# Kernel optimization log

Hardware: AMD Instinct MI355X
Metric: run time of the kernel (lower is better)

The kernel has to match this reference:

```python
import jax, jax.numpy as jnp
import numpy as np

LOG_EPS = 1e-30
MIN_EPS = 1e-8
N_CLASS = 19
GAMMA = 1.0        # focal_gamma
ADAPT_B = 0.2
ADAPT_A = 0.9      # beta (a_decay == 0)
ADAPT_D = 8.0
CONF_THRESH = 0.8  # uda_confidence_thresh


def setup_inputs() -> dict:
    key = jax.random.key(0)
    k1, k2 = jax.random.split(key)
    N, C, H, W = 2, N_CLASS, 512, 1024
    logits_before = jax.random.normal(k1, (N, C, H, W), jnp.float32)
    logits_after = jax.random.normal(k2, (N, C, H, W), jnp.float32)
    cls_thresh = jnp.ones((N_CLASS,), jnp.float32) * CONF_THRESH
    return {"logits_before": logits_before, "logits_after": logits_after,
            "cls_thresh": cls_thresh}


def ias_thresh(conf, label, cls_thresh):
    # conf, label: [N,H,W] max-prob and argmax class per pixel
    conf_f = conf.reshape(-1)    # [T]
    label_f = label.reshape(-1)  # [T]

    def per_class(c, thr):
        # class-c confidences, others pushed to the end of the descending sort
        vals = jnp.where(label_f == c, conf_f, -jnp.inf)
        ext = jnp.concatenate([vals, thr[None]])  # append current threshold
        srt = -jnp.sort(-ext)                     # descending
        count = jnp.sum(label_f == c)
        # index = int(len_extend * adapt_b * thresh**adapt_d); len_extend = count+1
        idx = jnp.floor((count + 1).astype(jnp.float32) * ADAPT_B * thr ** ADAPT_D).astype(jnp.int32)
        return srt[idx]  # count==0 -> idx==0 -> picks thr (matches torch branch)

    return jax.vmap(per_class)(jnp.arange(N_CLASS), cls_thresh)


def reference(logits_before, logits_after, cls_thresh):
    pb = jax.nn.softmax(logits_before, axis=1)
    pa = jax.nn.softmax(logits_after, axis=1)
    pb_d = jax.lax.stop_gradient(pb)
    log_pb_d = jnp.log(pb_d + LOG_EPS)
    log_pa = jnp.log(pa + LOG_EPS)

    bma = 1.0 - pa  # focal_type == 1: ones_like(pb_d) - pa
    label = jnp.argmax(pb_d, axis=1)  # [N,H,W]
    conf = jnp.max(pb_d, axis=1)      # [N,H,W]
    # scatter(select_mask)+sum == gather the argmax channel
    sel_diff = jnp.take_along_axis(bma, label[:, None], axis=1)  # [N,1,H,W]

    loss_kldiv = pb_d * (log_pb_d - jnp.abs(sel_diff) ** GAMMA * log_pa)
    loss_entropy = -pb * jnp.log(pb + LOG_EPS)
    loss = jnp.sum(loss_kldiv + loss_entropy, axis=1)  # [N,H,W]

    tmp = ias_thresh(conf, label, cls_thresh)
    new_thresh = ADAPT_A * cls_thresh + (1.0 - ADAPT_A) * tmp
    new_thresh = jnp.where(new_thresh >= 1.0, 0.999, new_thresh)

    pix_thresh = new_thresh[label]           # [N,H,W]
    mask = conf > pix_thresh
    adapt_ratio = jnp.mean(mask.astype(jnp.float32))
    solid_ratio = jnp.mean((conf > CONF_THRESH).astype(jnp.float32))

    # loss[mask] -> clamp -> mean, expressed as a masked mean (jit-safe)
    num = jnp.sum(jnp.where(mask, jnp.maximum(loss, MIN_EPS), 0.0))
    den = jnp.maximum(jnp.sum(mask).astype(loss.dtype), 1.0)
    return num / den, adapt_ratio, solid_ratio
```

## Files before the change

### kernel.cpp

```cpp
#include <hip/hip_runtime.h>
#include <math.h>

#define NCLS 19
#define HW   (512*1024)
#define CHW  (NCLS*HW)
#define TPIX (2*HW)
#define NB   512
#define NPART 32
#define CAND_MAX 4096
#define SUBB 1024
#define SCAP 256

#define WS_PART   0
#define WS_CANDC  622592
#define WS_ACCUM  622720
#define WS_DONE   622784
#define WS_SEL    622848
#define WS_NEWTH  623360
#define WS_CONF   623616
#define WS_LOSS   4817920
#define WS_LABEL  9012224
#define WS_CAND   10060800

#define TILE 256
__global__ __launch_bounds__(256)
void k1_pixel(const float* __restrict__ lb_t, const float* __restrict__ la_t,
              float* __restrict__ conf_o, float* __restrict__ loss_o,
              unsigned char* __restrict__ label_o,
              unsigned int* __restrict__ cand_cnt,
              unsigned int* __restrict__ accum_u,
              unsigned int* __restrict__ done)
{
    __shared__ float smem[2 * NCLS * TILE];
    const int tid = threadIdx.x;
    if (blockIdx.x == 0) {
        if (tid < NCLS)            cand_cnt[tid] = 0u;
        else if (tid < NCLS + 3)   accum_u[tid - NCLS] = 0u;
        else if (tid < NCLS + 6)   done[tid - NCLS - 3] = 0u;
    }
    const int wave = tid >> 6, lane = tid & 63;
    const int tb  = blockIdx.x * TILE;
    const int n   = tb >> 19;
    const int rem = tb & (HW - 1);
    const float* lb = lb_t + (size_t)n * CHW + rem;
    const float* la = la_t + (size_t)n * CHW + rem;

#pragma unroll
    for (int i = 0; i < 10; ++i) {
        int r = wave + 4 * i;
        if (r < 2 * NCLS) {
            const float* src = (r < NCLS) ? (lb + (size_t)r * HW)
                                          : (la + (size_t)(r - NCLS) * HW);
            __builtin_amdgcn_global_load_lds(
                (__attribute__((address_space(1))) void*)(src + (lane << 2)),
                (__attribute__((address_space(3))) void*)(smem + r * TILE),
                16, 0, 0);
        }
    }
    asm volatile("s_waitcnt vmcnt(0)" ::: "memory");
    __syncthreads();

    const int pix = tb + tid;
    float mb, zb, dot, a_lab, ma, za; int lab;
    {
        float bb = smem[tid];
        float aa = smem[NCLS * TILE + tid];
        mb = bb; zb = 1.0f; dot = aa; lab = 0; a_lab = aa; ma = aa; za = 1.0f;
    }
#pragma unroll
    for (int c = 1; c < NCLS; ++c) {
        float b = smem[c * TILE + tid];
        float a = smem[(NCLS + c) * TILE + tid];
        float mn = fmaxf(mb, b);
        float eo = __expf(mb - mn);
        float en = __expf(b - mn);
        zb  = zb * eo + en;
        dot = dot * eo + en * a;
        bool upd = b > mb;
        lab   = upd ? c : lab;
        a_lab = upd ? a : a_lab;
        mb = mn;
        float mna = fmaxf(ma, a);
        za = za * __expf(ma - mna) + __expf(a - mna);
        ma = mna;
    }

    float cf = 1.0f / zb;
    float pa_lab = __expf(a_lab - ma) / za;
    float ls = (1.0f - pa_lab) * (ma + __logf(za) - dot / zb);

    conf_o[pix]  = cf;
    loss_o[pix]  = ls;
    label_o[pix] = (unsigned char)lab;
}

__global__ __launch_bounds__(512)
void k2_hist(const float4* __restrict__ conf, const uchar4* __restrict__ label,
             unsigned short* __restrict__ part)
{
    __shared__ unsigned int lh[NCLS * NB];
    const int t = threadIdx.x;
    for (int w = t; w < NCLS * NB; w += 512) lh[w] = 0u;
    __syncthreads();

    const int per4  = TPIX / 4 / NPART;
    const int base4 = blockIdx.x * per4;
    for (int i = 0; i < per4 / 512; ++i) {
        int g = base4 + i * 512 + t;
        float4 c4 = conf[g];
        uchar4 l4 = label[g];
        float cf[4] = {c4.x, c4.y, c4.z, c4.w};
        int   lb[4] = {l4.x, l4.y, l4.z, l4.w};
#pragma unroll
        for (int k = 0; k < 4; ++k) {
            int bin = (int)(cf[k] * (float)NB);
            bin = bin < (NB - 1) ? bin : (NB - 1);
            atomicAdd(&lh[lb[k] * NB + bin], 1u);
        }
    }
    __syncthreads();

    unsigned short* dst = part + blockIdx.x * (NCLS * NB);
    for (int w = t; w < NCLS * NB; w += 512) dst[w] = (unsigned short)lh[w];
}

__global__ __launch_bounds__(256)
void k2_select(const unsigned short* __restrict__ part, const float* __restrict__ cls_thresh,
               int* __restrict__ sel, unsigned int* __restrict__ cand_cnt,
               float* __restrict__ cand)
{
    int c = blockIdx.x;
    int t = threadIdx.x;
    float thr = cls_thresh[c];
    int thr_bin = (int)(thr * (float)NB); thr_bin = thr_bin < (NB-1) ? thr_bin : (NB-1);

    int base = NB - (t + 1) * 2;
    unsigned h0 = 0, h1 = 0;
#pragma unroll 8
    for (int b = 0; b < NPART; ++b) {
        const unsigned short* p = part + b * (NCLS * NB) + c * NB;
        h0 += p[base];
        h1 += p[base + 1];
    }
    if (base == thr_bin)     h0 += 1u;
    if (base + 1 == thr_bin) h1 += 1u;
    unsigned s = h0 + h1;

    __shared__ unsigned sc[256];
    sc[t] = s;
    __syncthreads();
    for (int off = 1; off < 256; off <<= 1) {
        unsigned vt = sc[t];
        unsigned vp = (t >= off) ? sc[t - off] : 0u;
        __syncthreads();
        sc[t] = vt + vp;
        __syncthreads();
    }
    unsigned total_ext = sc[255];
    unsigned cnt = total_ext - 1u;
    int idx = (int)floorf((float)(cnt + 1u) * 0.2f * powf(thr, 8.0f));

    unsigned above = sc[t] - s;
    if ((unsigned)idx >= above && (unsigned)idx < above + s) {
        int B, r;
        if ((unsigned)idx < above + h1) { B = base + 1; r = (int)((unsigned)idx - above); }
        else                            { B = base;     r = (int)((unsigned)idx - above - h1); }
        sel[2 * c]     = B;
        sel[2 * c + 1] = r;
        if (B == thr_bin) {
            unsigned pos = atomicAdd(&cand_cnt[c], 1u);
            if (pos < CAND_MAX) cand[c * CAND_MAX + pos] = thr;
        }
    }
}

__global__ __launch_bounds__(256)
void k3_gather(const float4* __restrict__ conf, const uchar4* __restrict__ label,
               const int* __restrict__ sel, unsigned int* __restrict__ cand_cnt,
               float* __restrict__ cand)
{
    int g = blockIdx.x * 256 + threadIdx.x;
    float4 c4 = conf[g];
    uchar4 l4 = label[g];
    float cf[4] = {c4.x, c4.y, c4.z, c4.w};
    int   lb[4] = {l4.x, l4.y, l4.z, l4.w};
#pragma unroll
    for (int i = 0; i < 4; ++i) {
        int bin = (int)(cf[i] * (float)NB);
        bin = bin < (NB - 1) ? bin : (NB - 1);
        if (bin == sel[2 * lb[i]]) {
            unsigned pos = atomicAdd(&cand_cnt[lb[i]], 1u);
            if (pos < CAND_MAX) cand[lb[i] * CAND_MAX + pos] = cf[i];
        }
    }
}

__global__ __launch_bounds__(256)
void k4_thresh(const int* __restrict__ sel, const unsigned int* __restrict__ cand_cnt,
               const float* __restrict__ cand, const float* __restrict__ cls_thresh,
               float* __restrict__ newth)
{
    __shared__ unsigned int subh[SUBB];
    __shared__ float        sbuf[SCAP];
    __shared__ unsigned int scnt;
    __shared__ int          sS;
    __shared__ unsigned int sR2;
    __shared__ float        sres;

    const int c = blockIdx.x;
    const int t = threadIdx.x;
    unsigned mc = cand_cnt[c];
    int m = (int)(mc < (unsigned)CAND_MAX ? mc : (unsigned)CAND_MAX);
    int B = sel[2 * c];
    int r = sel[2 * c + 1];
    const float* v = cand + c * CAND_MAX;
    const float scale = (float)NB;

    for (int i = t; i < SUBB; i += 256) subh[i] = 0u;
    if (t == 0) { scnt = 0u; sS = 0; sR2 = 0u; sres = 0.0f; }
    __syncthreads();

    for (int i = t; i < m; i += 256) {
        float x = v[i];
        int s = (int)((x * scale - (float)B) * (float)SUBB);
        s = s < 0 ? 0 : (s > SUBB - 1 ? SUBB - 1 : s);
        atomicAdd(&subh[s], 1u);
    }
    __syncthreads();

    if (t < 64) {
        int lane = t;
        int cb = SUBB - 16 * (lane + 1);
        unsigned hsum = 0;
        for (int i = 0; i < 16; ++i) hsum += subh[cb + i];
        unsigned incl = hsum;
        for (int off = 1; off < 64; off <<= 1) {
            unsigned q = __shfl_up(incl, off, 64);
            if (lane >= off) incl += q;
        }
        unsigned above = incl - hsum;
        if ((unsigned)r >= above && (unsigned)r < above + hsum) {
            unsigned cum = above;
            for (int i = 15; i >= 0; --i) {
                unsigned h = subh[cb + i];
                if ((unsigned)r < cum + h) { sS = cb + i; sR2 = (unsigned)r - cum; break; }
                cum += h;
            }
        }
    }
    __syncthreads();
    const int S = sS;
    const unsigned r2 = sR2;

    for (int i = t; i < m; i += 256) {
        float x = v[i];
        int s = (int)((x * scale - (float)B) * (float)SUBB);
        s = s < 0 ? 0 : (s > SUBB - 1 ? SUBB - 1 : s);
        if (s == S) {
            unsigned p = atomicAdd(&scnt, 1u);
            if (p < (unsigned)SCAP) sbuf[p] = x;
        }
    }
    __syncthreads();
    unsigned cntS = scnt;

    if (cntS <= (unsigned)SCAP) {
        for (int i = t; i < (int)cntS; i += 256) {
            float x = sbuf[i];
            int gc = 0, e = 0;
            for (int j = 0; j < (int)cntS; ++j) {
                float y = sbuf[j];
                gc += (y > x); e += (y == x);
            }
            if (gc <= (int)r2 && (int)r2 < gc + e) sres = x;
        }
    } else {
        for (int i = t; i < m; i += 256) {
            float x = v[i];
            int s = (int)((x * scale - (float)B) * (float)SUBB);
            s = s < 0 ? 0 : (s > SUBB - 1 ? SUBB - 1 : s);
            if (s != S) continue;
            int gc = 0, e = 0;
            for (int j = 0; j < m; ++j) {
                float y = v[j];
                int sj = (int)((y * scale - (float)B) * (float)SUBB);
                sj = sj < 0 ? 0 : (sj > SUBB - 1 ? SUBB - 1 : sj);
                if (sj != S) continue;
                gc += (y > x); e += (y == x);
            }
            if (gc <= (int)r2 && (int)r2 < gc + e) sres = x;
        }
    }
    __syncthreads();
    if (t == 0) {
        float thr = cls_thresh[c];
        float nt = 0.9f * thr + 0.1f * sres;
        if (nt >= 1.0f) nt = 0.999f;
        newth[c] = nt;
    }
}

__global__ __launch_bounds__(256)
void k5_reduce_out(const float4* __restrict__ conf, const float4* __restrict__ loss,
                   const uchar4* __restrict__ label, const float* __restrict__ newth,
                   float* __restrict__ accum, unsigned int* __restrict__ done,
                   float* __restrict__ out)
{
    __shared__ float th[NCLS];
    if (threadIdx.x < NCLS) th[threadIdx.x] = newth[threadIdx.x];
    __syncthreads();

    int g = blockIdx.x * 256 + threadIdx.x;
    float4 c4 = conf[g];
    float4 s4 = loss[g];
    uchar4 l4 = label[g];
    float cf[4] = {c4.x, c4.y, c4.z, c4.w};
    float lv[4] = {s4.x, s4.y, s4.z, s4.w};
    int   lb[4] = {l4.x, l4.y, l4.z, l4.w};

    float ls = 0.0f; int mask = 0, solid = 0;
#pragma unroll
    for (int i = 0; i < 4; ++i) {
        bool m = cf[i] > th[lb[i]];
        mask  += m ? 1 : 0;
        solid += (cf[i] > 0.8f) ? 1 : 0;
        ls    += m ? fmaxf(lv[i], 1e-8f) : 0.0f;
    }
    for (int off = 32; off > 0; off >>= 1) {
        ls    += __shfl_down(ls, off, 64);
        mask  += __shfl_down(mask, off, 64);
        solid += __shfl_down(solid, off, 64);
    }
    __shared__ float s_ls[4];
    __shared__ int   s_m[4], s_s[4];
    int w = threadIdx.x >> 6;
    if ((threadIdx.x & 63) == 0) { s_ls[w] = ls; s_m[w] = mask; s_s[w] = solid; }
    __syncthreads();
    __shared__ int s_last;
    if (threadIdx.x == 0) {
        float L = s_ls[0] + s_ls[1] + s_ls[2] + s_ls[3];
        int   M = s_m[0] + s_m[1] + s_m[2] + s_m[3];
        int   S = s_s[0] + s_s[1] + s_s[2] + s_s[3];
        atomicAdd(&accum[0], L);
        atomicAdd(&((unsigned int*)accum)[1], (unsigned)M);
        atomicAdd(&((unsigned int*)accum)[2], (unsigned)S);
        __threadfence();
        s_last = (atomicAdd(&done[0], 1u) == (unsigned)(gridDim.x - 1)) ? 1 : 0;
    }
    __syncthreads();
    if (!s_last) return;
    if (threadIdx.x == 0) {
        __threadfence();
        float sum = accum[0];
        unsigned cm = ((const unsigned int*)accum)[1];
        unsigned cs = ((const unsigned int*)accum)[2];
        out[0] = sum / fmaxf((float)cm, 1.0f);
        out[1] = (float)cm / (float)TPIX;
        out[2] = (float)cs / (float)TPIX;
    }
}

extern "C" void kernel_launch(void* const* d_in, const int* in_sizes, int n_in,
                              void* d_out, int out_size, void* d_ws, size_t ws_size,
                              hipStream_t stream)
{
    const float* lb  = (const float*)d_in[0];
    const float* la  = (const float*)d_in[1];
    const float* cth = (const float*)d_in[2];
    float* out = (float*)d_out;

    char* ws = (char*)d_ws;
    unsigned short* part     = (unsigned short*)(ws + WS_PART);
    unsigned int*   cand_cnt = (unsigned int*)(ws + WS_CANDC);
    float*          accum    = (float*)(ws + WS_ACCUM);
    unsigned int*   done     = (unsigned int*)(ws + WS_DONE);
    int*            sel      = (int*)(ws + WS_SEL);
    float*          newth    = (float*)(ws + WS_NEWTH);
    float*          conf     = (float*)(ws + WS_CONF);
    float*          loss     = (float*)(ws + WS_LOSS);
    unsigned char*  label    = (unsigned char*)(ws + WS_LABEL);
    float*          cand     = (float*)(ws + WS_CAND);

    dim3 grd1(TPIX / TILE);
    dim3 grd4(TPIX / 4 / 256);

    k1_pixel<<<grd1, dim3(256), 0, stream>>>(lb, la, conf, loss, label,
                                             cand_cnt, (unsigned int*)accum, done);
    k2_hist<<<NPART, dim3(512), 0, stream>>>((const float4*)conf, (const uchar4*)label, part);
    k2_select<<<NCLS, dim3(256), 0, stream>>>(part, cth, sel, cand_cnt, cand);
    k3_gather<<<grd4, dim3(256), 0, stream>>>((const float4*)conf, (const uchar4*)label,
                                              sel, cand_cnt, cand);
    k4_thresh<<<NCLS, dim3(256), 0, stream>>>(sel, cand_cnt, cand, cth, newth);
    k5_reduce_out<<<grd4, dim3(256), 0, stream>>>((const float4*)conf, (const float4*)loss,
                                                  (const uchar4*)label, newth, accum, done, out);
}
```

Before: 247.8 us.

## Double-buffer k1 channel loads in chunks and widen blocks to 512 threads

Rewrites the per-pixel softmax/loss kernel so logits stream into LDS in five-channel chunks through a double buffer. The next chunk's async global-to-LDS loads overlap the online-softmax compute on the current chunk. Tiles grow to 512 pixels per 512-thread block while LDS per block stays about the same, which raises the number of resident pixels per CU. This adds extra barriers and split waits, and the counter-reset code now clears one fewer 'done' slot.

```diff
diff --git a/kernel.cpp b/kernel.cpp
--- a/kernel.cpp
+++ b/kernel.cpp
@@ -22,8 +22,12 @@
 #define WS_LABEL  9012224
 #define WS_CAND   10060800
 
-#define TILE 256
-__global__ __launch_bounds__(256)
+#define AS1 __attribute__((address_space(1)))
+#define AS3 __attribute__((address_space(3)))
+
+#define TILE 512
+#define CHUNK 5
+__global__ __launch_bounds__(512, 8)
 void k1_pixel(const float* __restrict__ lb_t, const float* __restrict__ la_t,
               float* __restrict__ conf_o, float* __restrict__ loss_o,
               unsigned char* __restrict__ label_o,
@@ -31,64 +35,96 @@
               unsigned int* __restrict__ accum_u,
               unsigned int* __restrict__ done)
 {
-    __shared__ float smem[2 * NCLS * TILE];
+    __shared__ float buf[2][2][CHUNK][TILE];
     const int tid = threadIdx.x;
     if (blockIdx.x == 0) {
         if (tid < NCLS)            cand_cnt[tid] = 0u;
         else if (tid < NCLS + 3)   accum_u[tid - NCLS] = 0u;
-        else if (tid < NCLS + 6)   done[tid - NCLS - 3] = 0u;
+        else if (tid < NCLS + 5)   done[tid - NCLS - 3] = 0u;
     }
     const int wave = tid >> 6, lane = tid & 63;
     const int tb  = blockIdx.x * TILE;
     const int n   = tb >> 19;
     const int rem = tb & (HW - 1);
-    const float* lb = lb_t + (size_t)n * CHW + rem;
-    const float* la = la_t + (size_t)n * CHW + rem;
-
-#pragma unroll
-    for (int i = 0; i < 10; ++i) {
-        int r = wave + 4 * i;
-        if (r < 2 * NCLS) {
-            const float* src = (r < NCLS) ? (lb + (size_t)r * HW)
-                                          : (la + (size_t)(r - NCLS) * HW);
+    const float* base0 = lb_t + (size_t)n * CHW + rem;
+    const float* base1 = la_t + (size_t)n * CHW + rem;
+
+    auto issue5 = [&](int ck, int cur) {
+#pragma unroll
+        for (int j = 0; j < 3; ++j) {
+            int d = wave + 8 * j;
+            if (d < 20) {
+                int t  = d >= 10;
+                int r  = t ? d - 10 : d;
+                int ch = r >> 1, h = r & 1;
+                const float* src = (t ? base1 : base0)
+                                 + (size_t)(ck * CHUNK + ch) * HW + h * 256 + (lane << 2);
+                __builtin_amdgcn_global_load_lds(
+                    (AS1 void*)src, (AS3 void*)&buf[cur][t][ch][h * 256], 16, 0, 0);
+            }
+        }
+    };
+    auto issue4 = [&]() {
+#pragma unroll
+        for (int j = 0; j < 2; ++j) {
+            int d = wave + 8 * j;
+            int t  = d >= 8;
+            int r  = t ? d - 8 : d;
+            int ch = r >> 1, h = r & 1;
+            const float* src = (t ? base1 : base0)
+                             + (size_t)(15 + ch) * HW + h * 256 + (lane << 2);
             __builtin_amdgcn_global_load_lds(
-                (__attribute__((address_space(1))) void*)(src + (lane << 2)),
-                (__attribute__((address_space(3))) void*)(smem + r * TILE),
-                16, 0, 0);
-        }
-    }
+                (AS1 void*)src, (AS3 void*)&buf[1][t][ch][h * 256], 16, 0, 0);
+        }
+    };
+
+    float mb = -INFINITY, ma = -INFINITY;
+    float zb = 0.0f, za = 0.0f, dot = 0.0f, a_lab = 0.0f;
+    int lab = -1;
+    auto compute = [&](int cur, int ck, int nch) {
+#pragma unroll
+        for (int i = 0; i < CHUNK; ++i) {
+            if (i >= nch) break;
+            float b = buf[cur][0][i][tid];
+            float a = buf[cur][1][i][tid];
+            int c = ck * CHUNK + i;
+            float mn = fmaxf(mb, b);
+            float eo = __expf(mb - mn);
+            float en = __expf(b - mn);
+            zb  = zb * eo + en;
+            dot = dot * eo + en * a;
+            bool upd = b > mb;
+            lab   = upd ? c : lab;
+            a_lab = upd ? a : a_lab;
+            mb = mn;
+            float mna = fmaxf(ma, a);
+            za = za * __expf(ma - mna) + __expf(a - mna);
+            ma = mna;
+        }
+    };
+
+    issue5(0, 0);
     asm volatile("s_waitcnt vmcnt(0)" ::: "memory");
-    __syncthreads();
-
-    const int pix = tb + tid;
-    float mb, zb, dot, a_lab, ma, za; int lab;
-    {
-        float bb = smem[tid];
-        float aa = smem[NCLS * TILE + tid];
-        mb = bb; zb = 1.0f; dot = aa; lab = 0; a_lab = aa; ma = aa; za = 1.0f;
-    }
-#pragma unroll
-    for (int c = 1; c < NCLS; ++c) {
-        float b = smem[c * TILE + tid];
-        float a = smem[(NCLS + c) * TILE + tid];
-        float mn = fmaxf(mb, b);
-        float eo = __expf(mb - mn);
-        float en = __expf(b - mn);
-        zb  = zb * eo + en;
-        dot = dot * eo + en * a;
-        bool upd = b > mb;
-        lab   = upd ? c : lab;
-        a_lab = upd ? a : a_lab;
-        mb = mn;
-        float mna = fmaxf(ma, a);
-        za = za * __expf(ma - mna) + __expf(a - mna);
-        ma = mna;
-    }
+    __builtin_amdgcn_s_barrier();
+    issue5(1, 1);
+    compute(0, 0, CHUNK);
+    asm volatile("s_waitcnt vmcnt(0)" ::: "memory");
+    __builtin_amdgcn_s_barrier();
+    issue5(2, 0);
+    compute(1, 1, CHUNK);
+    asm volatile("s_waitcnt vmcnt(0)" ::: "memory");
+    __builtin_amdgcn_s_barrier();
+    issue4();
+    compute(0, 2, CHUNK);
+    asm volatile("s_waitcnt vmcnt(0)" ::: "memory");
+    __builtin_amdgcn_s_barrier();
+    compute(1, 3, 4);
 
     float cf = 1.0f / zb;
     float pa_lab = __expf(a_lab - ma) / za;
     float ls = (1.0f - pa_lab) * (ma + __logf(za) - dot / zb);
 
+    const int pix = tb + tid;
     conf_o[pix]  = cf;
     loss_o[pix]  = ls;
     label_o[pix] = (unsigned char)lab;
@@ -384,7 +420,7 @@
     dim3 grd1(TPIX / TILE);
     dim3 grd4(TPIX / 4 / 256);
 
-    k1_pixel<<<grd1, dim3(256), 0, stream>>>(lb, la, conf, loss, label,
+    k1_pixel<<<grd1, dim3(512), 0, stream>>>(lb, la, conf, loss, label,
                                              cand_cnt, (unsigned int*)accum, done);
     k2_hist<<<NPART, dim3(512), 0, stream>>>((const float4*)conf, (const uchar4*)label, part);
     k2_select<<<NCLS, dim3(256), 0, stream>>>(part, cth, sel, cand_cnt, cand);
```

Measured after the change: 248.9 us. Within noise of the previous version (+0.4%).

## Process four pixels per thread with register double-buffered float4 channel loads

Applied to the files above, without the earlier changes.

The pixel kernel stops staging both logit tensors through LDS with global_load_lds. Each thread now handles four adjacent pixels with float4 loads and keeps two register buffers of four channels each, so the next chunk of loads is in flight while the current one is processed. Outputs are written as float4/uchar4 vectors and the grid shrinks by a factor of four. This adds register pressure, which launch_bounds(256,4) constrains, and leaves fewer blocks to hide memory latency. The init of the done counter also changes from three words to two, which could matter if the third word is used.

```diff
diff --git a/kernel.cpp b/kernel.cpp
--- a/kernel.cpp
+++ b/kernel.cpp
@@ -22,8 +22,8 @@
 #define WS_LABEL  9012224
 #define WS_CAND   10060800
 
-#define TILE 256
-__global__ __launch_bounds__(256)
+#define CH_STRIDE4 (HW/4)
+__global__ __launch_bounds__(256, 4)
 void k1_pixel(const float* __restrict__ lb_t, const float* __restrict__ la_t,
               float* __restrict__ conf_o, float* __restrict__ loss_o,
               unsigned char* __restrict__ label_o,
@@ -31,67 +31,103 @@
               unsigned int* __restrict__ accum_u,
               unsigned int* __restrict__ done)
 {
-    __shared__ float smem[2 * NCLS * TILE];
     const int tid = threadIdx.x;
     if (blockIdx.x == 0) {
         if (tid < NCLS)            cand_cnt[tid] = 0u;
         else if (tid < NCLS + 3)   accum_u[tid - NCLS] = 0u;
-        else if (tid < NCLS + 6)   done[tid - NCLS - 3] = 0u;
-    }
-    const int wave = tid >> 6, lane = tid & 63;
-    const int tb  = blockIdx.x * TILE;
-    const int n   = tb >> 19;
-    const int rem = tb & (HW - 1);
-    const float* lb = lb_t + (size_t)n * CHW + rem;
-    const float* la = la_t + (size_t)n * CHW + rem;
-
+        else if (tid < NCLS + 5)   done[tid - NCLS - 3] = 0u;
+    }
+    const int g    = blockIdx.x * 256 + tid;
+    const int pix0 = g << 2;
+    const int n    = pix0 >> 19;
+    const int rem  = pix0 & (HW - 1);
+    const float4* bb = (const float4*)(lb_t + (size_t)n * CHW + rem);
+    const float4* ab = (const float4*)(la_t + (size_t)n * CHW + rem);
+
+    float mb[4], zb[4], dot[4], ma[4], za[4], a_lab[4];
+    int lab[4];
 #pragma unroll
-    for (int i = 0; i < 10; ++i) {
-        int r = wave + 4 * i;
-        if (r < 2 * NCLS) {
-            const float* src = (r < NCLS) ? (lb + (size_t)r * HW)
-                                          : (la + (size_t)(r - NCLS) * HW);
-            __builtin_amdgcn_global_load_lds(
-                (__attribute__((address_space(1))) void*)(src + (lane << 2)),
-                (__attribute__((address_space(3))) void*)(smem + r * TILE),
-                16, 0, 0);
-        }
-    }
-    asm volatile("s_waitcnt vmcnt(0)" ::: "memory");
-    __syncthreads();
-
-    const int pix = tb + tid;
-    float mb, zb, dot, a_lab, ma, za; int lab;
-    {
-        float bb = smem[tid];
-        float aa = smem[NCLS * TILE + tid];
-        mb = bb; zb = 1.0f; dot = aa; lab = 0; a_lab = aa; ma = aa; za = 1.0f;
-    }
+    for (int j = 0; j < 4; ++j) {
+        mb[j] = -INFINITY; ma[j] = -INFINITY;
+        zb[j] = 0.0f; za[j] = 0.0f; dot[j] = 0.0f; a_lab[j] = 0.0f; lab[j] = -1;
+    }
+
+    float4 bA0, bA1, bA2, bA3, aA0, aA1, aA2, aA3;
+    float4 bB0, bB1, bB2, bB3, aB0, aB1, aB2, aB3;
+
+#define LOADA(c0, NC)                                                          \
+    do {                                                                       \
+        bA0 = bb[(size_t)(c0 + 0) * CH_STRIDE4];                               \
+        aA0 = ab[(size_t)(c0 + 0) * CH_STRIDE4];                               \
+        if (NC > 1) { bA1 = bb[(size_t)(c0 + 1) * CH_STRIDE4];                 \
+                      aA1 = ab[(size_t)(c0 + 1) * CH_STRIDE4]; }               \
+        if (NC > 2) { bA2 = bb[(size_t)(c0 + 2) * CH_STRIDE4];                 \
+                      aA2 = ab[(size_t)(c0 + 2) * CH_STRIDE4]; }               \
+        if (NC > 3) { bA3 = bb[(size_t)(c0 + 3) * CH_STRIDE4];                 \
+                      aA3 = ab[(size_t)(c0 + 3) * CH_STRIDE4]; }               \
+        __builtin_amdgcn_sched_barrier(0);                                     \
+    } while (0)
+#define LOADB(c0, NC)                                                          \
+    do {                                                                       \
+        bB0 = bb[(size_t)(c0 + 0) * CH_STRIDE4];                               \
+        aB0 = ab[(size_t)(c0 + 0) * CH_STRIDE4];                               \
+        if (NC > 1) { bB1 = bb[(size_t)(c0 + 1) * CH_STRIDE4];                 \
+                      aB1 = ab[(size_t)(c0 + 1) * CH_STRIDE4]; }               \
+        if (NC > 2) { bB2 = bb[(size_t)(c0 + 2) * CH_STRIDE4];                 \
+                      aB2 = ab[(size_t)(c0 + 2) * CH_STRIDE4]; }               \
+        if (NC > 3) { bB3 = bb[(size_t)(c0 + 3) * CH_STRIDE4];                 \
+                      aB3 = ab[(size_t)(c0 + 3) * CH_STRIDE4]; }               \
+        __builtin_amdgcn_sched_barrier(0);                                     \
+    } while (0)
+
+#define STEP(c, bv, av)                                                        \
+    do {                                                                       \
+        _Pragma("unroll")                                                      \
+        for (int j = 0; j < 4; ++j) {                                          \
+            float b = ((const float*)&(bv))[j];                                \
+            float a = ((const float*)&(av))[j];                                \
+            float mn = fmaxf(mb[j], b);                                        \
+            float eo = __expf(mb[j] - mn);       \
+            float en = __expf(b - mn);                                         \
+            zb[j]  = zb[j] * eo + en;                                          \
+            dot[j] = dot[j] * eo + en * a;                                     \
+            bool upd = b > mb[j];               \
+            lab[j]   = upd ? (c) : lab[j];                                     \
+            a_lab[j] = upd ? a : a_lab[j];                                     \
+            mb[j] = mn;                                                        \
+            float mna = fmaxf(ma[j], a);                                       \
+            za[j] = za[j] * __expf(ma[j] - mna) + __expf(a - mna);             \
+            ma[j] = mna;                                                       \
+        }                                                                      \
+    } while (0)
+
+    LOADA(0, 4);
+    LOADB(4, 4);
+    STEP(0, bA0, aA0); STEP(1, bA1, aA1); STEP(2, bA2, aA2); STEP(3, bA3, aA3);
+    LOADA(8, 4);
+    STEP(4, bB0, aB0); STEP(5, bB1, aB1); STEP(6, bB2, aB2); STEP(7, bB3, aB3);
+    LOADB(12, 4);
+    STEP(8, bA0, aA0); STEP(9, bA1, aA1); STEP(10, bA2, aA2); STEP(11, bA3, aA3);
+    LOADA(16, 3);
+    STEP(12, bB0, aB0); STEP(13, bB1, aB1); STEP(14, bB2, aB2); STEP(15, bB3, aB3);
+    STEP(16, bA0, aA0); STEP(17, bA1, aA1); STEP(18, bA2, aA2);
+
+    float4 cf4, ls4; uchar4 lb4;
 #pragma unroll
-    for (int c = 1; c < NCLS; ++c) {
-        float b = smem[c * TILE + tid];
-        float a = smem[(NCLS + c) * TILE + tid];
-        float mn = fmaxf(mb, b);
-        float eo = __expf(mb - mn);
-        float en = __expf(b - mn);
-        zb  = zb * eo + en;
-        dot = dot * eo + en * a;
-        bool upd = b > mb;
-        lab   = upd ? c : lab;
-        a_lab = upd ? a : a_lab;
-        mb = mn;
-        float mna = fmaxf(ma, a);
-        za = za * __expf(ma - mna) + __expf(a - mna);
-        ma = mna;
-    }
-
-    float cf = 1.0f / zb;
-    float pa_lab = __expf(a_lab - ma) / za;
-    float ls = (1.0f - pa_lab) * (ma + __logf(za) - dot / zb);
-
-    conf_o[pix]  = cf;
-    loss_o[pix]  = ls;
-    label_o[pix] = (unsigned char)lab;
+    for (int j = 0; j < 4; ++j) {
+        float cf = 1.0f / zb[j];
+        float pa_lab = __expf(a_lab[j] - ma[j]) / za[j];
+        float ls = (1.0f - pa_lab) * (ma[j] + __logf(za[j]) - dot[j] / zb[j]);
+        ((float*)&cf4)[j] = cf;
+        ((float*)&ls4)[j] = ls;
+        ((unsigned char*)&lb4)[j] = (unsigned char)lab[j];
+    }
+    ((float4*)conf_o)[g] = cf4;
+    ((float4*)loss_o)[g] = ls4;
+    ((uchar4*)label_o)[g] = lb4;
+#undef LOADA
+#undef LOADB
+#undef STEP
 }
 
 __global__ __launch_bounds__(512)
@@ -381,7 +417,7 @@
     unsigned char*  label    = (unsigned char*)(ws + WS_LABEL);
     float*          cand     = (float*)(ws + WS_CAND);
 
-    dim3 grd1(TPIX / TILE);
+    dim3 grd1(TPIX / 4 / 256);
     dim3 grd4(TPIX / 4 / 256);
 
     k1_pixel<<<grd1, dim3(256), 0, stream>>>(lb, la, conf, loss, label,
```

Result: no change. 251.0 us (+1.3%).
